# Kernel optimization log

Hardware: AMD Instinct MI355X
Metric: run time of the kernel (lower is better)

## Reference

```python
import jax, jax.numpy as jnp
import numpy as np

N_QUBITS = 8
N_WORDS = 16
DEGREE = 3
N_ANSATZ_LAYERS = 2
VOCAB = 50257
EMB = 512
BATCH = 16
N_ROTS = 4 * N_QUBITS * N_ANSATZ_LAYERS  # 64
DIM = 2 ** N_QUBITS


def _ry_mat(th):
    # [[cos, -sin],[sin, cos]] on theta/2, batched over leading dim
    c = jnp.cos(th / 2).astype(jnp.complex64)
    s = jnp.sin(th / 2).astype(jnp.complex64)
    return jnp.stack([jnp.stack([c, -s], -1), jnp.stack([s, c], -1)], -2)


def _rx_mat(th):
    # [[cos, -i sin],[-i sin, cos]] on theta/2
    c = jnp.cos(th / 2).astype(jnp.complex64)
    s = jnp.sin(th / 2).astype(jnp.complex64)
    return jnp.stack([jnp.stack([c, -1j * s], -1), jnp.stack([-1j * s, c], -1)], -2)


def _apply_1q(st, M, w):
    # st: [BB, 2^n] complex, M: [BB,2,2]; wire 0 is the most-significant axis (tq convention)
    BB = st.shape[0]
    s = st.reshape(BB, 2 ** w, 2, -1)
    s = jnp.einsum('bij,bljr->blir', M, s)
    return s.reshape(BB, -1)


def _apply_ctrl(st, M, c, t, n):
    # controlled-1q gate: apply M on target t only in the control=1 subspace
    BB = st.shape[0]
    full = st.reshape((BB,) + (2,) * n)
    s0 = jnp.take(full, 0, axis=c + 1)
    s1 = jnp.take(full, 1, axis=c + 1)
    ta = (t if t < c else t - 1) + 1  # target axis after removing control axis
    s1 = jnp.moveaxis(s1, ta, -1)
    s1 = jnp.einsum('bij,b...j->b...i', M, s1)
    s1 = jnp.moveaxis(s1, -1, ta)
    return jnp.stack([s0, s1], axis=c + 1).reshape(BB, -1)


def _sim14(st, params, n, layers):
    # circuit-14 ansatz: ry ring, crx down-ring, ry ring, crx up-ring (per layer)
    idx = 0
    for _ in range(layers):
        for i in range(n):
            st = _apply_1q(st, _ry_mat(params[:, idx]), i); idx += 1
        for i in range(n - 1, -1, -1):
            st = _apply_ctrl(st, _rx_mat(params[:, idx]), i, (i + 1) % n, n); idx += 1
        for i in range(n):
            st = _apply_1q(st, _ry_mat(params[:, idx]), i); idx += 1
        for i in [n - 1] + list(range(n - 1)):
            st = _apply_ctrl(st, _rx_mat(params[:, idx]), i, (i - 1) % n, n); idx += 1
    return st


def _apply_unitaries(base, wparams, coeffs):
    # base: [B, DIM]; wparams: [B, W, N_ROTS]; coeffs: [B, W] complex -> LCU sum_w c_w U_w |psi>
    B, W = wparams.shape[0], wparams.shape[1]
    rep = jnp.repeat(base, W, axis=0)  # matches torch repeat(1,W).view(-1,DIM)
    st = _sim14(rep, wparams.reshape(B * W, -1), N_QUBITS, N_ANSATZ_LAYERS)
    return jnp.einsum('bwi,bw->bi', st.reshape(B, W, DIM), coeffs)


def _measure_xyz(st, n):
    # Pauli X/Y/Z expectations per wire; order: [x_0..x_{n-1}, y_..., z_...]
    BB = st.shape[0]
    xs, ys, zs = [], [], []
    for w in range(n):
        s = st.reshape(BB, 2 ** w, 2, -1)
        a0, a1 = s[:, :, 0, :], s[:, :, 1, :]
        cross = jnp.sum(jnp.conj(a0) * a1, axis=(1, 2))
        xs.append(2 * jnp.real(cross))
        ys.append(2 * jnp.imag(cross))
        zs.append(jnp.sum(jnp.abs(a0) ** 2 - jnp.abs(a1) ** 2, axis=(1, 2)))
    return jnp.concatenate([jnp.stack(xs, -1), jnp.stack(ys, -1), jnp.stack(zs, -1)], axis=-1)


def reference(x, embedding_W, emb2rot_W, emb2rot_b, poly_coeffs, mix_coeffs_ri, qff_params, ff1_W, ff1_b, ff2_W, ff2_b):
    B = x.shape[0]
    mix = (mix_coeffs_ri[:, 0] + 1j * mix_coeffs_ri[:, 1]).astype(jnp.complex64)
    coeffs = mix / jnp.maximum(jnp.sum(jnp.abs(mix)), 1e-12)  # L1 normalize
    coeffs = jnp.broadcast_to(coeffs[None, :], (B, N_WORDS))
    emb = embedding_W[x]                       # [B, W, EMB]
    wparams = emb @ emb2rot_W.T + emb2rot_b    # [B, W, N_ROTS]; dropout is identity in eval
    base = jnp.zeros((B, DIM), jnp.complex64).at[:, 0].set(1.0)
    acc = poly_coeffs[0] * base
    work = base
    for d in range(1, DEGREE + 1):
        work = _apply_unitaries(work, wparams, coeffs)
        acc = acc + poly_coeffs[d] * work
    mixed = acc / jnp.sum(jnp.abs(poly_coeffs))
    final_probs = jnp.linalg.norm(mixed, axis=-1)
    normed = mixed / jnp.maximum(final_probs, 1e-12)[:, None]
    qp = jnp.broadcast_to(qff_params[None, :4 * N_QUBITS], (B, 4 * N_QUBITS))  # qff uses 1 layer
    st = _sim14(normed, qp, N_QUBITS, 1)
    exps = _measure_xyz(st, N_QUBITS)          # [B, 3*n_qubits]
    h = jax.nn.relu(exps @ ff1_W.T + ff1_b)
    op = h @ ff2_W.T + ff2_b
    return op, jnp.mean(final_probs)


def setup_inputs():
    key = jax.random.key(0)
    ks = jax.random.split(key, 12)
    x = jax.random.randint(ks[0], (BATCH, N_WORDS), 0, VOCAB)
    embedding_W = jax.random.normal(ks[1], (VOCAB, EMB), jnp.float32) * 0.02
    emb2rot_W = jax.random.normal(ks[2], (N_ROTS, EMB), jnp.float32) * (1.0 / np.sqrt(EMB))
    emb2rot_b = jax.random.normal(ks[3], (N_ROTS,), jnp.float32) * 0.01
    poly_coeffs = jax.random.uniform(ks[4], (DEGREE + 1,), jnp.float32)
    mix_coeffs_ri = jax.random.uniform(ks[5], (N_WORDS, 2), jnp.float32)
    qff_params = jax.random.uniform(ks[6], (N_ROTS,), jnp.float32)
    NM = 3 * N_QUBITS
    ff1_W = jax.random.normal(ks[7], (EMB, NM), jnp.float32) * (1.0 / np.sqrt(NM))
    ff1_b = jnp.zeros((EMB,), jnp.float32)
    ff2_W = jax.random.normal(ks[8], (VOCAB, EMB), jnp.float32) * (1.0 / np.sqrt(EMB))
    ff2_b = jnp.zeros((VOCAB,), jnp.float32)
    return {"x": x, "embedding_W": embedding_W, "emb2rot_W": emb2rot_W, "emb2rot_b": emb2rot_b,
            "poly_coeffs": poly_coeffs, "mix_coeffs_ri": mix_coeffs_ri, "qff_params": qff_params,
            "ff1_W": ff1_W, "ff1_b": ff1_b, "ff2_W": ff2_W, "ff2_b": ff2_b}
```

## Files before the change

kernel.cpp:

```cpp
#include <hip/hip_runtime.h>
#include <hip/hip_bf16.h>

#define NQ 8
#define DIM 256
#define NB 16
#define NW 16
#define VOCABN 50257
#define EMBN 512
#define NTILES ((VOCABN + 15) / 16)

typedef __attribute__((ext_vector_type(8))) short short8;
typedef __attribute__((ext_vector_type(4))) float f32x4;

__device__ __forceinline__ float2 shfl2(float2 a, int m){
  float2 r; r.x = __shfl_xor(a.x, m, 64); r.y = __shfl_xor(a.y, m, 64); return r;
}
__device__ __forceinline__ float wave_sum(float x){
  #pragma unroll
  for (int off = 1; off < 64; off <<= 1) x += __shfl_xor(x, off, 64);
  return x;
}
__device__ __forceinline__ short f2bf(float f){
  __hip_bfloat16 h = __float2bfloat16(f);
  return __builtin_bit_cast(short, h);
}

__device__ __forceinline__ void ry_pair(float2& a0, float2& a1, float c, float s){
  float2 n0 = make_float2(c*a0.x - s*a1.x, c*a0.y - s*a1.y);
  float2 n1 = make_float2(s*a0.x + c*a1.x, s*a0.y + c*a1.y);
  a0 = n0; a1 = n1;
}
__device__ __forceinline__ void rx_pair(float2& a0, float2& a1, float c, float s){
  float2 n0 = make_float2(c*a0.x + s*a1.y, c*a0.y - s*a1.x);
  float2 n1 = make_float2(c*a1.x + s*a0.y, c*a1.y - s*a0.x);
  a0 = n0; a1 = n1;
}

__device__ __forceinline__ void apply_gate(float2 v[4], int lane, int kind, int cbit, int tbit,
                                           float c, float s){
  if (kind == 0){
    if (tbit == 7){ ry_pair(v[0], v[2], c, s); ry_pair(v[1], v[3], c, s); }
    else if (tbit == 6){ ry_pair(v[0], v[1], c, s); ry_pair(v[2], v[3], c, s); }
    else {
      int m = 1 << tbit;
      #pragma unroll
      for (int r = 0; r < 4; ++r){
        float2 w = shfl2(v[r], m);
        float sg = (lane & m) ? s : -s;
        v[r] = make_float2(c*v[r].x + sg*w.x, c*v[r].y + sg*w.y);
      }
    }
  } else {
    if (tbit >= 6){
      if (cbit >= 6){
        if (cbit == 7) rx_pair(v[2], v[3], c, s);
        else           rx_pair(v[1], v[3], c, s);
      } else {
        int cm = 1 << cbit;
        if (lane & cm){
          if (tbit == 7){ rx_pair(v[0], v[2], c, s); rx_pair(v[1], v[3], c, s); }
          else          { rx_pair(v[0], v[1], c, s); rx_pair(v[2], v[3], c, s); }
        }
      }
    } else {
      int m = 1 << tbit;
      if (cbit >= 6){
        int r0 = (cbit == 6) ? 1 : 2;
        float2 w0 = shfl2(v[r0], m);
        float2 w1 = shfl2(v[3], m);
        v[r0] = make_float2(c*v[r0].x + s*w0.y, c*v[r0].y - s*w0.x);
        v[3]  = make_float2(c*v[3].x  + s*w1.y, c*v[3].y  - s*w1.x);
      } else {
        int cm = 1 << cbit;
        bool act = (lane & cm) != 0;
        #pragma unroll
        for (int r = 0; r < 4; ++r){
          float2 w = shfl2(v[r], m);
          if (act) v[r] = make_float2(c*v[r].x + s*w.y, c*v[r].y - s*w.x);
        }
      }
    }
  }
}

__device__ __forceinline__ void sim32(float2 v[4], int lane, const float2* __restrict__ cs){
  constexpr int KIND[32] = {0,0,0,0,0,0,0,0, 1,1,1,1,1,1,1,1, 0,0,0,0,0,0,0,0, 1,1,1,1,1,1,1,1};
  constexpr int CB[32]   = {0,0,0,0,0,0,0,0, 0,1,2,3,4,5,6,7, 0,0,0,0,0,0,0,0, 0,7,6,5,4,3,2,1};
  constexpr int TB[32]   = {7,6,5,4,3,2,1,0, 7,0,1,2,3,4,5,6, 7,6,5,4,3,2,1,0, 1,0,7,6,5,4,3,2};
  #pragma unroll
  for (int g = 0; g < 32; ++g){
    float2 p = cs[g];
    apply_gate(v, lane, KIND[g], CB[g], TB[g], p.x, p.y);
  }
}

__device__ __forceinline__ void measure_one(const float2 v[4], int lane, int t,
                                            float& xr, float& xi, float& zz){
  xr = 0.f; xi = 0.f; zz = 0.f;
  if (t == 7){
    #pragma unroll
    for (int r = 0; r < 2; ++r){
      float2 a0 = v[r], a1 = v[r+2];
      xr += a0.x*a1.x + a0.y*a1.y;
      xi += a0.x*a1.y - a0.y*a1.x;
      zz += (a0.x*a0.x + a0.y*a0.y) - (a1.x*a1.x + a1.y*a1.y);
    }
  } else if (t == 6){
    #pragma unroll
    for (int r = 0; r < 4; r += 2){
      float2 a0 = v[r], a1 = v[r+1];
      xr += a0.x*a1.x + a0.y*a1.y;
      xi += a0.x*a1.y - a0.y*a1.x;
      zz += (a0.x*a0.x + a0.y*a0.y) - (a1.x*a1.x + a1.y*a1.y);
    }
  } else {
    int m = 1 << t;
    #pragma unroll
    for (int r = 0; r < 4; ++r){
      float2 a = v[r];
      float2 w = shfl2(a, m);
      if (!(lane & m)){
        xr += a.x*w.x + a.y*w.y;
        xi += a.x*w.y - a.y*w.x;
        zz += (a.x*a.x + a.y*a.y) - (w.x*w.x + w.y*w.y);
      }
    }
  }
  xr = wave_sum(xr); xi = wave_sum(xi); zz = wave_sum(zz);
}

__global__ __launch_bounds__(64) void k_pd1(
    const int* __restrict__ x, const float* __restrict__ embW,
    const float* __restrict__ e2rW, const float* __restrict__ e2rb,
    const float* __restrict__ mixri, const float* __restrict__ qff,
    float* __restrict__ wcs, float* __restrict__ qcs, float2* __restrict__ S1)
{
  const int p = blockIdx.x;
  const int j = threadIdx.x;
  __shared__ float2 cs[64];

  {
    const int tok = x[p];
    const float4* er = (const float4*)(embW + (size_t)tok * EMBN);
    const float4* wr = (const float4*)(e2rW + (size_t)j * EMBN);
    float acc = e2rb[j];
    #pragma unroll 4
    for (int k = 0; k < EMBN/4; ++k){
      float4 e = er[k], w4 = wr[k];
      acc += e.x*w4.x + e.y*w4.y + e.z*w4.z + e.w*w4.w;
    }
    float th = 0.5f * acc;
    float2 c2 = make_float2(cosf(th), sinf(th));
    cs[j] = c2;
    ((float2*)wcs)[p*64 + j] = c2;
    if (p == 0 && j < 32){ float t = 0.5f * qff[j]; ((float2*)qcs)[j] = make_float2(cosf(t), sinf(t)); }
  }
  __syncthreads();

  const int lane = j;
  float2 v[4];
  v[0] = make_float2(lane == 0 ? 1.f : 0.f, 0.f);
  v[1] = v[2] = v[3] = make_float2(0.f, 0.f);
  sim32(v, lane, cs);
  sim32(v, lane, cs + 32);

  float ssum = 0.f;
  #pragma unroll
  for (int i = 0; i < 16; ++i){
    float mr = mixri[2*i], mi = mixri[2*i+1];
    ssum += sqrtf(mr*mr + mi*mi);
  }
  ssum = fmaxf(ssum, 1e-12f);
  const int w = p & 15;
  const float2 coef = make_float2(mixri[2*w]/ssum, mixri[2*w+1]/ssum);
  #pragma unroll
  for (int r = 0; r < 4; ++r){
    float2 a = v[r];
    S1[p*DIM + ((r<<6) | lane)] = make_float2(coef.x*a.x - coef.y*a.y, coef.x*a.y + coef.y*a.x);
  }
}

__global__ __launch_bounds__(64) void k_deg(
    const float2* __restrict__ Sin, float2* __restrict__ Sout,
    const float* __restrict__ wcs, const float* __restrict__ mixri,
    const float* __restrict__ poly, float2* __restrict__ accs, int dprev)
{
  const int p = blockIdx.x, lane = threadIdx.x;
  const int b = p >> 4, w = p & 15;
  float2 v[4];
  v[0] = v[1] = v[2] = v[3] = make_float2(0.f, 0.f);
  const float2* base = Sin + b*NW*DIM;
  #pragma unroll
  for (int ww = 0; ww < NW; ++ww){
    #pragma unroll
    for (int r = 0; r < 4; ++r){
      float2 a = base[ww*DIM + ((r<<6) | lane)];
      v[r].x += a.x; v[r].y += a.y;
    }
  }
  if (w == 0){
    const float pd = poly[dprev];
    #pragma unroll
    for (int r = 0; r < 4; ++r){
      const int idx = (r<<6) | lane;
      float2 cur = make_float2(pd*v[r].x, pd*v[r].y);
      if (dprev == 1){
        if (idx == 0) cur.x += poly[0];
        accs[b*DIM + idx] = cur;
      } else {
        float2 old = accs[b*DIM + idx];
        accs[b*DIM + idx] = make_float2(old.x + cur.x, old.y + cur.y);
      }
    }
  }
  const float2* mycs = ((const float2*)wcs) + p*64;
  sim32(v, lane, mycs);
  sim32(v, lane, mycs + 32);
  float ssum = 0.f;
  #pragma unroll
  for (int i = 0; i < 16; ++i){
    float mr = mixri[2*i], mi = mixri[2*i+1];
    ssum += sqrtf(mr*mr + mi*mi);
  }
  ssum = fmaxf(ssum, 1e-12f);
  const float2 coef = make_float2(mixri[2*w]/ssum, mixri[2*w+1]/ssum);
  #pragma unroll
  for (int r = 0; r < 4; ++r){
    float2 a = v[r];
    Sout[p*DIM + ((r<<6) | lane)] = make_float2(coef.x*a.x - coef.y*a.y, coef.x*a.y + coef.y*a.x);
  }
}

__global__ __launch_bounds__(512) void k_final(
    const float2* __restrict__ Sin, const float2* __restrict__ accs,
    const float* __restrict__ poly, const float* __restrict__ qcs,
    const float* __restrict__ ff1W, const float* __restrict__ ff1b,
    __hip_bfloat16* __restrict__ hbf, float* __restrict__ fprobs)
{
  const int b = blockIdx.x, tid = threadIdx.x;
  const int w = tid >> 6, lane = tid & 63;
  __shared__ float2 work[DIM];
  __shared__ float  red[8];
  __shared__ float  exps[24];
  __shared__ float  inv_s;
  __shared__ float  ff1_lds[EMBN*24];

  {
    const float4* f4 = (const float4*)ff1W;
    float4* d4 = (float4*)ff1_lds;
    #pragma unroll
    for (int i = 0; i < 6; ++i) d4[i*512 + tid] = f4[i*512 + tid];
  }
  const float psum = fabsf(poly[0]) + fabsf(poly[1]) + fabsf(poly[2]) + fabsf(poly[3]);
  float ssl = 0.f;
  if (tid < DIM){
    float2 s = make_float2(0.f, 0.f);
    const float2* base = Sin + b*NW*DIM;
    #pragma unroll
    for (int ww = 0; ww < NW; ++ww){ float2 a = base[ww*DIM + tid]; s.x += a.x; s.y += a.y; }
    float2 ac = accs[b*DIM + tid];
    const float p3 = poly[3];
    s = make_float2((ac.x + p3*s.x)/psum, (ac.y + p3*s.y)/psum);
    work[tid] = s;
    ssl = s.x*s.x + s.y*s.y;
  }
  ssl = wave_sum(ssl);
  if (lane == 0) red[w] = ssl;
  __syncthreads();
  if (tid == 0){
    float fp = sqrtf(red[0] + red[1] + red[2] + red[3]);
    fprobs[b] = fp;
    inv_s = 1.f / fmaxf(fp, 1e-12f);
  }
  __syncthreads();
  {
    const float inv = inv_s;
    float2 v[4];
    #pragma unroll
    for (int r = 0; r < 4; ++r){
      float2 m = work[(r<<6) | lane];
      v[r] = make_float2(m.x*inv, m.y*inv);
    }
    sim32(v, lane, (const float2*)qcs);
    float xr, xi, zz;
    measure_one(v, lane, 7 - w, xr, xi, zz);
    if (lane == 0){ exps[w] = 2.f*xr; exps[8+w] = 2.f*xi; exps[16+w] = zz; }
  }
  __syncthreads();
  float a = ff1b[tid];
  const float* wr = ff1_lds + tid*24;
  #pragma unroll
  for (int m2 = 0; m2 < 24; ++m2) a += exps[m2]*wr[m2];
  hbf[b*EMBN + tid] = __float2bfloat16(fmaxf(a, 0.f));
}

__global__ __launch_bounds__(256) void k_out(
    const __hip_bfloat16* __restrict__ hbf, const float* __restrict__ ff2W,
    const float* __restrict__ ff2b, const float* __restrict__ fprobs,
    float* __restrict__ out)
{
  const int tid = threadIdx.x;
  const int w = tid >> 6, lane = tid & 63;
  const int tile = blockIdx.x*4 + w;

  if (blockIdx.x == 0 && tid == 0){
    float s = 0.f;
    #pragma unroll
    for (int i = 0; i < 16; ++i) s += fprobs[i];
    out[(size_t)NB*VOCABN] = s * (1.f/16.f);
  }

  const int n = lane & 15;
  const int quad = lane >> 4;

  short8 bfrag[16];
  {
    const short* hb = (const short*)hbf + n*EMBN;
    #pragma unroll
    for (int f = 0; f < 16; ++f)
      bfrag[f] = *(const short8*)(hb + f*32 + quad*8);
  }

  if (tile >= NTILES) return;
  const int tbase = tile * 16;
  int row = tbase + n; if (row > VOCABN-1) row = VOCABN-1;
  const float* ar = ff2W + (size_t)row * EMBN + quad*8;

  f32x4 acc = {0.f, 0.f, 0.f, 0.f};
  #pragma unroll
  for (int f = 0; f < 16; ++f){
    float4 a0 = *(const float4*)(ar + f*32);
    float4 a1 = *(const float4*)(ar + f*32 + 4);
    short8 af;
    af[0] = f2bf(a0.x); af[1] = f2bf(a0.y); af[2] = f2bf(a0.z); af[3] = f2bf(a0.w);
    af[4] = f2bf(a1.x); af[5] = f2bf(a1.y); af[6] = f2bf(a1.z); af[7] = f2bf(a1.w);
    acc = __builtin_amdgcn_mfma_f32_16x16x32_bf16(af, bfrag[f], acc, 0, 0, 0);
  }

  #pragma unroll
  for (int r = 0; r < 4; ++r){
    const int v = tbase + quad*4 + r;
    if (v < VOCABN)
      out[(size_t)n*VOCABN + v] = acc[r] + ff2b[v];
  }
}

extern "C" void kernel_launch(void* const* d_in, const int* in_sizes, int n_in,
                              void* d_out, int out_size, void* d_ws, size_t ws_size,
                              hipStream_t stream)
{
  const int*   x     = (const int*)  d_in[0];
  const float* embW  = (const float*)d_in[1];
  const float* e2rW  = (const float*)d_in[2];
  const float* e2rb  = (const float*)d_in[3];
  const float* poly  = (const float*)d_in[4];
  const float* mixri = (const float*)d_in[5];
  const float* qff   = (const float*)d_in[6];
  const float* ff1W  = (const float*)d_in[7];
  const float* ff1b  = (const float*)d_in[8];
  const float* ff2W  = (const float*)d_in[9];
  const float* ff2b  = (const float*)d_in[10];
  float* out = (float*)d_out;
  float* ws  = (float*)d_ws;

  float*  wcs    = ws;
  float*  qcs    = ws + 32768;
  __hip_bfloat16* hbf = (__hip_bfloat16*)(ws + 32832);
  float*  fprobs = ws + 36928;
  float2* accs   = (float2*)(ws + 36944);
  float2* S1     = (float2*)(ws + 45136);
  float2* S2     = (float2*)(ws + 176208);

  k_pd1  <<<256, 64, 0, stream>>>(x, embW, e2rW, e2rb, mixri, qff, wcs, qcs, S1);
  k_deg  <<<256, 64, 0, stream>>>(S1, S2, wcs, mixri, poly, accs, 1);
  k_deg  <<<256, 64, 0, stream>>>(S2, S1, wcs, mixri, poly, accs, 2);
  k_final<<<NB, 512, 0, stream>>>(S1, accs, poly, qcs, ff1W, ff1b, hbf, fprobs);
  k_out  <<<(NTILES + 3)/4, 256, 0, stream>>>(hbf, ff2W, ff2b, fprobs, out);
}
```

Measured before the change: 278.0 us.

## Split reductions across four waves and coalesce output stores via LDS transpose

```diff
diff --git a/kernel.cpp b/kernel.cpp
--- a/kernel.cpp
+++ b/kernel.cpp
@@ -129,105 +129,135 @@
   xr = wave_sum(xr); xi = wave_sum(xi); zz = wave_sum(zz);
 }
 
-__global__ __launch_bounds__(64) void k_pd1(
+__global__ __launch_bounds__(256) void k_pd1(
     const int* __restrict__ x, const float* __restrict__ embW,
     const float* __restrict__ e2rW, const float* __restrict__ e2rb,
     const float* __restrict__ mixri, const float* __restrict__ qff,
     float* __restrict__ wcs, float* __restrict__ qcs, float2* __restrict__ S1)
 {
   const int p = blockIdx.x;
-  const int j = threadIdx.x;
+  const int t = threadIdx.x;
+  const int j = t & 63;
+  const int kq = t >> 6;
+  __shared__ float part[4][64];
   __shared__ float2 cs[64];
 
   {
     const int tok = x[p];
-    const float4* er = (const float4*)(embW + (size_t)tok * EMBN);
-    const float4* wr = (const float4*)(e2rW + (size_t)j * EMBN);
-    float acc = e2rb[j];
+    const float4* er = (const float4*)(embW + (size_t)tok * EMBN) + kq*32;
+    const float4* wr = (const float4*)(e2rW + (size_t)j * EMBN) + kq*32;
+    float acc = 0.f;
     #pragma unroll 4
-    for (int k = 0; k < EMBN/4; ++k){
+    for (int k = 0; k < 32; ++k){
       float4 e = er[k], w4 = wr[k];
       acc += e.x*w4.x + e.y*w4.y + e.z*w4.z + e.w*w4.w;
     }
-    float th = 0.5f * acc;
+    part[kq][j] = acc;
+  }
+  __syncthreads();
+
+  if (t < 64){
+    float a = part[0][j] + part[1][j] + part[2][j] + part[3][j] + e2rb[j];
+    float th = 0.5f * a;
     float2 c2 = make_float2(cosf(th), sinf(th));
     cs[j] = c2;
     ((float2*)wcs)[p*64 + j] = c2;
-    if (p == 0 && j < 32){ float t = 0.5f * qff[j]; ((float2*)qcs)[j] = make_float2(cosf(t), sinf(t)); }
-  }
-  __syncthreads();
-
-  const int lane = j;
-  float2 v[4];
-  v[0] = make_float2(lane == 0 ? 1.f : 0.f, 0.f);
-  v[1] = v[2] = v[3] = make_float2(0.f, 0.f);
-  sim32(v, lane, cs);
-  sim32(v, lane, cs + 32);
-
-  float ssum = 0.f;
-  #pragma unroll
-  for (int i = 0; i < 16; ++i){
-    float mr = mixri[2*i], mi = mixri[2*i+1];
-    ssum += sqrtf(mr*mr + mi*mi);
-  }
-  ssum = fmaxf(ssum, 1e-12f);
-  const int w = p & 15;
-  const float2 coef = make_float2(mixri[2*w]/ssum, mixri[2*w+1]/ssum);
-  #pragma unroll
-  for (int r = 0; r < 4; ++r){
-    float2 a = v[r];
-    S1[p*DIM + ((r<<6) | lane)] = make_float2(coef.x*a.x - coef.y*a.y, coef.x*a.y + coef.y*a.x);
-  }
-}
-
-__global__ __launch_bounds__(64) void k_deg(
+    if (p == 0 && j < 32){ float tq = 0.5f * qff[j]; ((float2*)qcs)[j] = make_float2(cosf(tq), sinf(tq)); }
+  }
+  __syncthreads();
+
+  if (t < 64){
+    const int lane = j;
+    float2 v[4];
+    v[0] = make_float2(lane == 0 ? 1.f : 0.f, 0.f);
+    v[1] = v[2] = v[3] = make_float2(0.f, 0.f);
+    sim32(v, lane, cs);
+    sim32(v, lane, cs + 32);
+
+    float ssum = 0.f;
+    #pragma unroll
+    for (int i = 0; i < 16; ++i){
+      float mr = mixri[2*i], mi = mixri[2*i+1];
+      ssum += sqrtf(mr*mr + mi*mi);
+    }
+    ssum = fmaxf(ssum, 1e-12f);
+    const int w = p & 15;
+    const float2 coef = make_float2(mixri[2*w]/ssum, mixri[2*w+1]/ssum);
+    #pragma unroll
+    for (int r = 0; r < 4; ++r){
+      float2 a = v[r];
+      S1[p*DIM + ((r<<6) | lane)] = make_float2(coef.x*a.x - coef.y*a.y, coef.x*a.y + coef.y*a.x);
+    }
+  }
+}
+
+__global__ __launch_bounds__(256) void k_deg(
     const float2* __restrict__ Sin, float2* __restrict__ Sout,
     const float* __restrict__ wcs, const float* __restrict__ mixri,
     const float* __restrict__ poly, float2* __restrict__ accs, int dprev)
 {
-  const int p = blockIdx.x, lane = threadIdx.x;
+  const int p = blockIdx.x, t = threadIdx.x;
   const int b = p >> 4, w = p & 15;
-  float2 v[4];
-  v[0] = v[1] = v[2] = v[3] = make_float2(0.f, 0.f);
-  const float2* base = Sin + b*NW*DIM;
-  #pragma unroll
-  for (int ww = 0; ww < NW; ++ww){
-    #pragma unroll
-    for (int r = 0; r < 4; ++r){
-      float2 a = base[ww*DIM + ((r<<6) | lane)];
-      v[r].x += a.x; v[r].y += a.y;
-    }
-  }
-  if (w == 0){
-    const float pd = poly[dprev];
+  const int lane = t & 63, wv = t >> 6;
+  __shared__ float2 part[4][DIM];
+
+  {
+    float2 v[4];
+    v[0] = v[1] = v[2] = v[3] = make_float2(0.f, 0.f);
+    const float2* base = Sin + b*NW*DIM;
+    #pragma unroll
+    for (int k = 0; k < 4; ++k){
+      const int ww = wv*4 + k;
+      #pragma unroll
+      for (int r = 0; r < 4; ++r){
+        float2 a = base[ww*DIM + ((r<<6) | lane)];
+        v[r].x += a.x; v[r].y += a.y;
+      }
+    }
+    #pragma unroll
+    for (int r = 0; r < 4; ++r) part[wv][(r<<6) | lane] = v[r];
+  }
+  __syncthreads();
+
+  if (t < 64){
+    float2 v[4];
     #pragma unroll
     for (int r = 0; r < 4; ++r){
       const int idx = (r<<6) | lane;
-      float2 cur = make_float2(pd*v[r].x, pd*v[r].y);
-      if (dprev == 1){
-        if (idx == 0) cur.x += poly[0];
-        accs[b*DIM + idx] = cur;
-      } else {
-        float2 old = accs[b*DIM + idx];
-        accs[b*DIM + idx] = make_float2(old.x + cur.x, old.y + cur.y);
-      }
-    }
-  }
-  const float2* mycs = ((const float2*)wcs) + p*64;
-  sim32(v, lane, mycs);
-  sim32(v, lane, mycs + 32);
-  float ssum = 0.f;
-  #pragma unroll
-  for (int i = 0; i < 16; ++i){
-    float mr = mixri[2*i], mi = mixri[2*i+1];
-    ssum += sqrtf(mr*mr + mi*mi);
-  }
-  ssum = fmaxf(ssum, 1e-12f);
-  const float2 coef = make_float2(mixri[2*w]/ssum, mixri[2*w+1]/ssum);
-  #pragma unroll
-  for (int r = 0; r < 4; ++r){
-    float2 a = v[r];
-    Sout[p*DIM + ((r<<6) | lane)] = make_float2(coef.x*a.x - coef.y*a.y, coef.x*a.y + coef.y*a.x);
+      float2 s0 = part[0][idx], s1 = part[1][idx], s2 = part[2][idx], s3 = part[3][idx];
+      v[r] = make_float2(s0.x+s1.x+s2.x+s3.x, s0.y+s1.y+s2.y+s3.y);
+    }
+    if (w == 0){
+      const float pd = poly[dprev];
+      #pragma unroll
+      for (int r = 0; r < 4; ++r){
+        const int idx = (r<<6) | lane;
+        float2 cur = make_float2(pd*v[r].x, pd*v[r].y);
+        if (dprev == 1){
+          if (idx == 0) cur.x += poly[0];
+          accs[b*DIM + idx] = cur;
+        } else {
+          float2 old = accs[b*DIM + idx];
+          accs[b*DIM + idx] = make_float2(old.x + cur.x, old.y + cur.y);
+        }
+      }
+    }
+    const float2* mycs = ((const float2*)wcs) + p*64;
+    sim32(v, lane, mycs);
+    sim32(v, lane, mycs + 32);
+    float ssum = 0.f;
+    #pragma unroll
+    for (int i = 0; i < 16; ++i){
+      float mr = mixri[2*i], mi = mixri[2*i+1];
+      ssum += sqrtf(mr*mr + mi*mi);
+    }
+    ssum = fmaxf(ssum, 1e-12f);
+    const float2 coef = make_float2(mixri[2*w]/ssum, mixri[2*w+1]/ssum);
+    #pragma unroll
+    for (int r = 0; r < 4; ++r){
+      float2 a = v[r];
+      Sout[p*DIM + ((r<<6) | lane)] = make_float2(coef.x*a.x - coef.y*a.y, coef.x*a.y + coef.y*a.x);
+    }
   }
 }
 
@@ -299,9 +329,10 @@
     const float* __restrict__ ff2b, const float* __restrict__ fprobs,
     float* __restrict__ out)
 {
+  __shared__ float tile[4][16][17];
   const int tid = threadIdx.x;
   const int w = tid >> 6, lane = tid & 63;
-  const int tile = blockIdx.x*4 + w;
+  const int tileid = blockIdx.x*4 + w;
 
   if (blockIdx.x == 0 && tid == 0){
     float s = 0.f;
@@ -321,8 +352,8 @@
       bfrag[f] = *(const short8*)(hb + f*32 + quad*8);
   }
 
-  if (tile >= NTILES) return;
-  const int tbase = tile * 16;
+  if (tileid >= NTILES) return;
+  const int tbase = tileid * 16;
   int row = tbase + n; if (row > VOCABN-1) row = VOCABN-1;
   const float* ar = ff2W + (size_t)row * EMBN + quad*8;
 
@@ -339,9 +370,26 @@
 
   #pragma unroll
   for (int r = 0; r < 4; ++r){
-    const int v = tbase + quad*4 + r;
-    if (v < VOCABN)
-      out[(size_t)n*VOCABN + v] = acc[r] + ff2b[v];
+    const int m = quad*4 + r;
+    const int v = tbase + m;
+    const float bias = ff2b[(v < VOCABN) ? v : (VOCABN-1)];
+    tile[w][n][m] = acc[r] + bias;
+  }
+  __builtin_amdgcn_wave_barrier();
+
+  const int n2 = lane >> 2;
+  const int mg = lane & 3;
+  const int v0 = tbase + mg*4;
+  if (tbase + 15 < VOCABN){
+    float4 o = make_float4(tile[w][n2][mg*4+0], tile[w][n2][mg*4+1],
+                           tile[w][n2][mg*4+2], tile[w][n2][mg*4+3]);
+    *(float4*)(out + (size_t)n2*VOCABN + v0) = o;
+  } else {
+    #pragma unroll
+    for (int k = 0; k < 4; ++k){
+      const int v = v0 + k;
+      if (v < VOCABN) out[(size_t)n2*VOCABN + v] = tile[w][n2][mg*4+k];
+    }
   }
 }
 
@@ -371,9 +419,9 @@
   float2* S1     = (float2*)(ws + 45136);
   float2* S2     = (float2*)(ws + 176208);
 
-  k_pd1  <<<256, 64, 0, stream>>>(x, embW, e2rW, e2rb, mixri, qff, wcs, qcs, S1);
-  k_deg  <<<256, 64, 0, stream>>>(S1, S2, wcs, mixri, poly, accs, 1);
-  k_deg  <<<256, 64, 0, stream>>>(S2, S1, wcs, mixri, poly, accs, 2);
+  k_pd1  <<<256, 256, 0, stream>>>(x, embW, e2rW, e2rb, mixri, qff, wcs, qcs, S1);
+  k_deg  <<<256, 256, 0, stream>>>(S1, S2, wcs, mixri, poly, accs, 1);
+  k_deg  <<<256, 256, 0, stream>>>(S2, S1, wcs, mixri, poly, accs, 2);
   k_final<<<NB, 512, 0, stream>>>(S1, accs, poly, qcs, ff1W, ff1b, hbf, fprobs);
   k_out  <<<(NTILES + 3)/4, 256, 0, stream>>>(hbf, ff2W, ff2b, fprobs, out);
 }
```

After: 263.9 us. 5.1% less time.
